# Kernel tuning notes

Measured on AMD Instinct MI355X. Metric: run time of the kernel, lower is better.

## Reference

```python
import jax, jax.numpy as jnp
import numpy as np

N, F, O = 8192, 1024, 1024
NUM_NEIGH = 10


def setup_inputs() -> dict:
    key = jax.random.key(0)
    k1, k2, k3, k4, k5 = jax.random.split(key, 5)
    X = jax.random.normal(k1, (N, F), dtype=jnp.float32)
    A = jax.random.uniform(k2, (N, N), dtype=jnp.float32)
    stdv = 1.0 / np.sqrt(O)
    W = jax.random.uniform(k3, (2 * F, O), dtype=jnp.float32, minval=-stdv, maxval=stdv)
    b = jax.random.uniform(k4, (O,), dtype=jnp.float32, minval=-stdv, maxval=stdv)
    # Uniform neighbor sampling (original uses np.random.choice over range(N) per node)
    sampled_idx = jax.random.randint(k5, (N, NUM_NEIGH), 0, N, dtype=jnp.int32)
    return {"X": X, "A": A, "W": W, "b": b, "sampled_idx": sampled_idx}


def reference(X, A, W, b, sampled_idx):
    # aggregate: mean of uniformly sampled neighbor features per node.
    # (The matrix_power of the normalized A in the original is dead code; A's
    #  values never influence the output.)
    gathered = X[sampled_idx]                 # [N, num_neigh, F]
    aggregated = jnp.mean(gathered, axis=1)   # [N, F]
    combined = jnp.concatenate([X, aggregated], axis=1)  # [N, 2F]
    return combined @ W + b                   # [N, O]
```

## Files before the change

kernel.cpp:

```cpp
#include <hip/hip_runtime.h>
#include <stdint.h>

#define NN 8192
#define FD 1024
#define OD 1024
#define KD 2048
#define NB 10

typedef short bf16x8 __attribute__((ext_vector_type(8)));
typedef float f32x4  __attribute__((ext_vector_type(4)));

static __device__ __forceinline__ float bf2f(ushort u) {
  union { uint32_t i; float f; } v; v.i = ((uint32_t)u) << 16; return v.f;
}
static __device__ __forceinline__ ushort f2bf(float f) {
  union { float f; uint32_t i; } v; v.f = f;
  uint32_t x = v.i;
  return (ushort)((x + 0x7FFFu + ((x >> 16) & 1u)) >> 16);
}
static __device__ __forceinline__ bf16x8 cvt8(const float* p) {
  const float4 a = *reinterpret_cast<const float4*>(p);
  const float4 b = *reinterpret_cast<const float4*>(p + 4);
  bf16x8 v;
  v[0] = (short)f2bf(a.x); v[1] = (short)f2bf(a.y);
  v[2] = (short)f2bf(a.z); v[3] = (short)f2bf(a.w);
  v[4] = (short)f2bf(b.x); v[5] = (short)f2bf(b.y);
  v[6] = (short)f2bf(b.z); v[7] = (short)f2bf(b.w);
  return v;
}

static __device__ __forceinline__ void async16(const ushort* g, ushort* l) {
  __builtin_amdgcn_global_load_lds(
      (const __attribute__((address_space(1))) uint32_t*)(const void*)g,
      (__attribute__((address_space(3))) uint32_t*)(void*)l, 16, 0, 0);
}

__global__ __launch_bounds__(256) void xconv(const float* __restrict__ X,
                                             ushort* __restrict__ Ab) {
  const int q   = blockIdx.x * 256 + threadIdx.x;
  const int row = q >> 7;
  const int col = (q & 127) * 8;
  const bf16x8 v = cvt8(X + (size_t)row * FD + col);
  *reinterpret_cast<bf16x8*>(Ab + (size_t)row * KD + col) = v;
}

__global__ __launch_bounds__(256) void aggk(const int* __restrict__ idx,
                                            ushort* __restrict__ Ab) {
  const int row  = blockIdx.x * 2 + (threadIdx.x >> 7);
  const int lane = threadIdx.x & 127;
  const int col  = lane * 8;
  const int* ip = idx + (size_t)row * NB;
  int nb[NB];
#pragma unroll
  for (int j = 0; j < NB; ++j) nb[j] = ip[j];
  float acc[8] = {0.f, 0.f, 0.f, 0.f, 0.f, 0.f, 0.f, 0.f};
#pragma unroll
  for (int j = 0; j < NB; ++j) {
    const uint4 v = *reinterpret_cast<const uint4*>(Ab + (size_t)nb[j] * KD + col);
    const ushort* u = reinterpret_cast<const ushort*>(&v);
#pragma unroll
    for (int e = 0; e < 8; ++e) acc[e] += bf2f(u[e]);
  }
  bf16x8 o;
#pragma unroll
  for (int e = 0; e < 8; ++e) o[e] = (short)f2bf(acc[e] * 0.1f);
  *reinterpret_cast<bf16x8*>(Ab + (size_t)row * KD + FD + col) = o;
}

__global__ __launch_bounds__(1024) void wconv(const float* __restrict__ W,
                                              ushort* __restrict__ Wtb) {
  __shared__ float tile[64][65];
  const int k0 = blockIdx.x * 64;
  const int n0 = blockIdx.y * 64;
  const int tx = threadIdx.x;
  const int ty = threadIdx.y;
#pragma unroll
  for (int r = 0; r < 4; ++r) {
    const int kl = ty + r * 16;
    tile[kl][tx] = W[(size_t)(k0 + kl) * OD + n0 + tx];
  }
  __syncthreads();
#pragma unroll
  for (int r = 0; r < 4; ++r) {
    const int nl = ty + r * 16;
    Wtb[(size_t)(n0 + nl) * KD + k0 + tx] = f2bf(tile[tx][nl]);
  }
}

__global__ __launch_bounds__(256, 2) void gemm_fast2(const ushort* __restrict__ Ab,
                                                     const ushort* __restrict__ Wtb,
                                                     const float* __restrict__ Bias,
                                                     float* __restrict__ Out) {
  __shared__ ushort lA[128 * 32];
  __shared__ ushort lB[128 * 32];
  const int t    = threadIdx.x;
  const int m0   = blockIdx.y * 128;
  const int n0   = blockIdx.x * 128;
  const int wave = t >> 6;
  const int lane = t & 63;
  const int wm   = (wave & 1) * 64;
  const int wn   = (wave >> 1) * 64;
  const int l15  = lane & 15;
  const int quad = lane >> 4;

  f32x4 acc[4][4];
#pragma unroll
  for (int i = 0; i < 4; ++i)
#pragma unroll
    for (int j = 0; j < 4; ++j) acc[i][j] = (f32x4){0.f, 0.f, 0.f, 0.f};

  const int row0 = t >> 2, ch = t & 3;
  const int row1 = (256 + t) >> 2;
  const ushort* gA0 = Ab  + (size_t)(m0 + row0) * KD + ch * 8;
  const ushort* gA1 = Ab  + (size_t)(m0 + row1) * KD + ch * 8;
  const ushort* gB0 = Wtb + (size_t)(n0 + row0) * KD + ch * 8;
  const ushort* gB1 = Wtb + (size_t)(n0 + row1) * KD + ch * 8;

  for (int k0 = 0; k0 < KD; k0 += 32) {
    async16(gA0 + k0, lA + t * 8);
    async16(gA1 + k0, lA + (256 + t) * 8);
    async16(gB0 + k0, lB + t * 8);
    async16(gB1 + k0, lB + (256 + t) * 8);
    __syncthreads();

    bf16x8 afr[4], bfr[4];
#pragma unroll
    for (int mi = 0; mi < 4; ++mi)
      afr[mi] = *reinterpret_cast<const bf16x8*>(lA + (wm + mi * 16 + l15) * 32 + quad * 8);
#pragma unroll
    for (int ni = 0; ni < 4; ++ni)
      bfr[ni] = *reinterpret_cast<const bf16x8*>(lB + (wn + ni * 16 + l15) * 32 + quad * 8);
#pragma unroll
    for (int mi = 0; mi < 4; ++mi)
#pragma unroll
      for (int ni = 0; ni < 4; ++ni)
        acc[mi][ni] = __builtin_amdgcn_mfma_f32_16x16x32_bf16(afr[mi], bfr[ni], acc[mi][ni], 0, 0, 0);
    __syncthreads();
  }

#pragma unroll
  for (int ni = 0; ni < 4; ++ni) {
    const int gn = n0 + wn + ni * 16 + l15;
    const float bv = Bias[gn];
#pragma unroll
    for (int mi = 0; mi < 4; ++mi) {
      const int gm = m0 + wm + mi * 16 + quad * 4;
#pragma unroll
      for (int r = 0; r < 4; ++r)
        Out[(size_t)(gm + r) * OD + gn] = acc[mi][ni][r] + bv;
    }
  }
}

__global__ __launch_bounds__(256) void gemm_fused(const float* __restrict__ X,
                                                  const float* __restrict__ W,
                                                  const float* __restrict__ Bias,
                                                  const int* __restrict__ idx,
                                                  float* __restrict__ Out) {
  __shared__ ushort lA[128 * 32];
  __shared__ ushort lB[32 * 128];
  const int t    = threadIdx.x;
  const int m0   = blockIdx.y * 128;
  const int n0   = blockIdx.x * 128;
  const int wave = t >> 6;
  const int lane = t & 63;
  const int wm   = (wave & 1) * 64;
  const int wn   = (wave >> 1) * 64;
  const int l15  = lane & 15;
  const int quad = lane >> 4;

  f32x4 acc[4][4];
#pragma unroll
  for (int i = 0; i < 4; ++i)
#pragma unroll
    for (int j = 0; j < 4; ++j) acc[i][j] = (f32x4){0.f, 0.f, 0.f, 0.f};

  for (int kt = 0; kt < KD / 32; ++kt) {
    const int k0 = kt * 32;
    if (k0 < FD) {
#pragma unroll
      for (int r = 0; r < 2; ++r) {
        const int q = r * 256 + t;
        const int row = q >> 2, ch = q & 3;
        *reinterpret_cast<bf16x8*>(lA + q * 8) =
            cvt8(X + (size_t)(m0 + row) * FD + k0 + ch * 8);
      }
    } else {
      const int kc = k0 - FD;
#pragma unroll
      for (int r = 0; r < 2; ++r) {
        const int q = r * 256 + t;
        const int row = q >> 2, ch = q & 3;
        float a8[8] = {0.f, 0.f, 0.f, 0.f, 0.f, 0.f, 0.f, 0.f};
        const int* ip = idx + (size_t)(m0 + row) * NB;
#pragma unroll
        for (int j = 0; j < NB; ++j) {
          const float* p = X + (size_t)ip[j] * FD + kc + ch * 8;
          const float4 a = *(const float4*)p;
          const float4 b = *(const float4*)(p + 4);
          a8[0] += a.x; a8[1] += a.y; a8[2] += a.z; a8[3] += a.w;
          a8[4] += b.x; a8[5] += b.y; a8[6] += b.z; a8[7] += b.w;
        }
        bf16x8 v;
#pragma unroll
        for (int e = 0; e < 8; ++e) v[e] = (short)f2bf(a8[e] * 0.1f);
        *reinterpret_cast<bf16x8*>(lA + q * 8) = v;
      }
    }
#pragma unroll
    for (int r = 0; r < 2; ++r) {
      const int q = r * 256 + t;
      const int kr = q >> 4, ch = q & 15;
      *reinterpret_cast<bf16x8*>(lB + q * 8) =
          cvt8(W + (size_t)(k0 + kr) * OD + n0 + ch * 8);
    }
    __syncthreads();

    bf16x8 afr[4], bfr[4];
#pragma unroll
    for (int mi = 0; mi < 4; ++mi)
      afr[mi] = *reinterpret_cast<const bf16x8*>(lA + (wm + mi * 16 + l15) * 32 + quad * 8);
#pragma unroll
    for (int ni = 0; ni < 4; ++ni) {
      const int col = wn + ni * 16 + l15;
#pragma unroll
      for (int j = 0; j < 8; ++j)
        bfr[ni][j] = (short)lB[(quad * 8 + j) * 128 + col];
    }
#pragma unroll
    for (int mi = 0; mi < 4; ++mi)
#pragma unroll
      for (int ni = 0; ni < 4; ++ni)
        acc[mi][ni] = __builtin_amdgcn_mfma_f32_16x16x32_bf16(afr[mi], bfr[ni], acc[mi][ni], 0, 0, 0);
    __syncthreads();
  }
#pragma unroll
  for (int ni = 0; ni < 4; ++ni) {
    const int gn = n0 + wn + ni * 16 + l15;
    const float bv = Bias[gn];
#pragma unroll
    for (int mi = 0; mi < 4; ++mi) {
      const int gm = m0 + wm + mi * 16 + quad * 4;
#pragma unroll
      for (int r = 0; r < 4; ++r)
        Out[(size_t)(gm + r) * OD + gn] = acc[mi][ni][r] + bv;
    }
  }
}

extern "C" void kernel_launch(void* const* d_in, const int* in_sizes, int n_in,
                              void* d_out, int out_size, void* d_ws, size_t ws_size,
                              hipStream_t stream) {
  const float* X   = (const float*)d_in[0];
  const float* W   = (const float*)d_in[2];
  const float* b   = (const float*)d_in[3];
  const int*   idx = (const int*)d_in[4];
  float* out = (float*)d_out;

  const size_t need = ((size_t)NN * KD + (size_t)OD * KD) * sizeof(ushort);
  if (ws_size >= need) {
    ushort* Ab  = (ushort*)d_ws;
    ushort* Wtb = Ab + (size_t)NN * KD;

    xconv<<<NN * FD / (256 * 8), 256, 0, stream>>>(X, Ab);
    wconv<<<dim3(KD / 64, OD / 64), dim3(64, 16), 0, stream>>>(W, Wtb);
    aggk<<<NN / 2, 256, 0, stream>>>(idx, Ab);
    gemm_fast2<<<dim3(OD / 128, NN / 128), 256, 0, stream>>>(Ab, Wtb, b, out);
  } else {
    gemm_fused<<<dim3(OD / 128, NN / 128), 256, 0, stream>>>(X, W, b, idx, out);
  }
}
```

Baseline: 402.4 us.

## Double K-tile depth, swizzle LDS layout, and remap blocks per XCD in GEMM

The GEMM now stages a 64-wide K slice per iteration instead of 32, which halves the number of barrier pairs. The LDS layout is XOR-style swizzled by row so that fragment reads avoid bank conflicts. Blocks use a 1D grid remapped so that consecutive blocks on the same XCD share A row tiles, which is meant to improve L2 reuse. LDS usage doubles, which may limit occupancy at two blocks per CU.

After: 389.9 us. 1.03x faster.

```diff
diff --git a/kernel.cpp b/kernel.cpp
--- a/kernel.cpp
+++ b/kernel.cpp
@@ -87,15 +87,19 @@
   }
 }
 
-__global__ __launch_bounds__(256, 2) void gemm_fast2(const ushort* __restrict__ Ab,
+__global__ __launch_bounds__(256, 2) void gemm_fast3(const ushort* __restrict__ Ab,
                                                      const ushort* __restrict__ Wtb,
                                                      const float* __restrict__ Bias,
                                                      float* __restrict__ Out) {
-  __shared__ ushort lA[128 * 32];
-  __shared__ ushort lB[128 * 32];
-  const int t    = threadIdx.x;
-  const int m0   = blockIdx.y * 128;
-  const int n0   = blockIdx.x * 128;
+  __shared__ ushort lA[128 * 64];
+  __shared__ ushort lB[128 * 64];
+  const int t  = threadIdx.x;
+  const int id  = blockIdx.x;
+  const int xcd = id & 7;
+  const int j   = id >> 3;
+  const int m0  = (xcd * 8 + (j >> 3)) * 128;
+  const int n0  = (j & 7) * 128;
+
   const int wave = t >> 6;
   const int lane = t & 63;
   const int wm   = (wave & 1) * 64;
@@ -107,34 +111,48 @@
 #pragma unroll
   for (int i = 0; i < 4; ++i)
 #pragma unroll
-    for (int j = 0; j < 4; ++j) acc[i][j] = (f32x4){0.f, 0.f, 0.f, 0.f};
-
-  const int row0 = t >> 2, ch = t & 3;
-  const int row1 = (256 + t) >> 2;
-  const ushort* gA0 = Ab  + (size_t)(m0 + row0) * KD + ch * 8;
-  const ushort* gA1 = Ab  + (size_t)(m0 + row1) * KD + ch * 8;
-  const ushort* gB0 = Wtb + (size_t)(n0 + row0) * KD + ch * 8;
-  const ushort* gB1 = Wtb + (size_t)(n0 + row1) * KD + ch * 8;
-
-  for (int k0 = 0; k0 < KD; k0 += 32) {
-    async16(gA0 + k0, lA + t * 8);
-    async16(gA1 + k0, lA + (256 + t) * 8);
-    async16(gB0 + k0, lB + t * 8);
-    async16(gB1 + k0, lB + (256 + t) * 8);
-    __syncthreads();
-
-    bf16x8 afr[4], bfr[4];
-#pragma unroll
-    for (int mi = 0; mi < 4; ++mi)
-      afr[mi] = *reinterpret_cast<const bf16x8*>(lA + (wm + mi * 16 + l15) * 32 + quad * 8);
-#pragma unroll
-    for (int ni = 0; ni < 4; ++ni)
-      bfr[ni] = *reinterpret_cast<const bf16x8*>(lB + (wn + ni * 16 + l15) * 32 + quad * 8);
-#pragma unroll
-    for (int mi = 0; mi < 4; ++mi)
-#pragma unroll
-      for (int ni = 0; ni < 4; ++ni)
-        acc[mi][ni] = __builtin_amdgcn_mfma_f32_16x16x32_bf16(afr[mi], bfr[ni], acc[mi][ni], 0, 0, 0);
+    for (int jj = 0; jj < 4; ++jj) acc[i][jj] = (f32x4){0.f, 0.f, 0.f, 0.f};
+
+  const ushort* gA[4];
+  const ushort* gB[4];
+#pragma unroll
+  for (int i = 0; i < 4; ++i) {
+    const int q   = i * 256 + t;
+    const int row = q >> 3;
+    const int ch  = q & 7;
+    const int c   = (ch - row) & 7;
+    gA[i] = Ab  + (size_t)(m0 + row) * KD + c * 8;
+    gB[i] = Wtb + (size_t)(n0 + row) * KD + c * 8;
+  }
+
+  for (int k0 = 0; k0 < KD; k0 += 64) {
+#pragma unroll
+    for (int i = 0; i < 4; ++i) {
+      async16(gA[i] + k0, lA + (i * 256 + t) * 8);
+      async16(gB[i] + k0, lB + (i * 256 + t) * 8);
+    }
+    __syncthreads();
+
+#pragma unroll
+    for (int s = 0; s < 2; ++s) {
+      const int c = s * 4 + quad;
+      bf16x8 afr[4], bfr[4];
+#pragma unroll
+      for (int mi = 0; mi < 4; ++mi) {
+        const int r = wm + mi * 16 + l15;
+        afr[mi] = *reinterpret_cast<const bf16x8*>(lA + r * 64 + ((c + r) & 7) * 8);
+      }
+#pragma unroll
+      for (int ni = 0; ni < 4; ++ni) {
+        const int r = wn + ni * 16 + l15;
+        bfr[ni] = *reinterpret_cast<const bf16x8*>(lB + r * 64 + ((c + r) & 7) * 8);
+      }
+#pragma unroll
+      for (int mi = 0; mi < 4; ++mi)
+#pragma unroll
+        for (int ni = 0; ni < 4; ++ni)
+          acc[mi][ni] = __builtin_amdgcn_mfma_f32_16x16x32_bf16(afr[mi], bfr[ni], acc[mi][ni], 0, 0, 0);
+    }
     __syncthreads();
   }
 
@@ -265,7 +283,7 @@
     xconv<<<NN * FD / (256 * 8), 256, 0, stream>>>(X, Ab);
     wconv<<<dim3(KD / 64, OD / 64), dim3(64, 16), 0, stream>>>(W, Wtb);
     aggk<<<NN / 2, 256, 0, stream>>>(idx, Ab);
-    gemm_fast2<<<dim3(OD / 128, NN / 128), 256, 0, stream>>>(Ab, Wtb, b, out);
+    gemm_fast3<<<512, 256, 0, stream>>>(Ab, Wtb, b, out);
   } else {
     gemm_fused<<<dim3(OD / 128, NN / 128), 256, 0, stream>>>(X, W, b, idx, out);
   }
```
